# Optimization experiments

Hardware: AMD Instinct MI355X
Metric: run time of the kernel (lower is better)

Reference implementation:

```python
import jax, jax.numpy as jnp
import numpy as np

B, S, D = 8, 2048, 512
EPS = float(jnp.finfo(jnp.float32).eps)  # torch RMSNorm eps=None -> finfo eps


def rmsnorm(x, w):
    var = jnp.mean(jnp.square(x), axis=-1, keepdims=True)
    return x * jax.lax.rsqrt(var + EPS) * w


def setup_inputs() -> dict:
    key = jax.random.key(0)
    ks = jax.random.split(key, 9)
    x = jax.random.normal(ks[0], (B, S, D), dtype=jnp.float32)
    q_expl = jax.random.normal(ks[1], (B, S, D), dtype=jnp.float32)
    k_expl = jax.random.normal(ks[2], (B, S, D), dtype=jnp.float32)
    # parameters (torch Linear: y = x @ W^T + b; store W already transposed [in, out])
    sc1 = 1.0 / np.sqrt(D)
    W1 = jax.random.uniform(ks[3], (D, 2 * D), jnp.float32, -sc1, sc1)
    b1 = jax.random.uniform(ks[4], (2 * D,), jnp.float32, -sc1, sc1)
    W2 = jax.random.uniform(ks[5], (D, D), jnp.float32, -sc1, sc1)
    b2 = jax.random.uniform(ks[6], (D,), jnp.float32, -sc1, sc1)
    norm1_w = jnp.ones((D,), jnp.float32)
    norm2_w = jnp.ones((D,), jnp.float32)
    return {"x": x, "q_expl": q_expl, "k_expl": k_expl,
            "W1": W1, "b1": b1, "W2": W2, "b2": b2,
            "norm1_w": norm1_w, "norm2_w": norm2_w}


def reference(x, q_expl, k_expl, W1, b1, W2, b2, norm1_w, norm2_w):
    d = x.shape[-1]
    # single-head attention: scores [B,S,S]
    scores = jnp.einsum('bqd,bkd->bqk', q_expl, k_expl) / jnp.sqrt(jnp.float32(d))
    attn = jax.nn.softmax(scores, axis=-1)
    attn_out = jnp.einsum('bqk,bkd->bqd', attn, x)
    # dropout is identity in eval mode
    h = rmsnorm(x + attn_out, norm1_w)
    # GeGLU FFN: Linear(D->2D), chunk, gelu(x1)*x2, Linear(D->D)
    proj = h @ W1 + b1
    x1, x2 = jnp.split(proj, 2, axis=-1)
    g = jax.nn.gelu(x1, approximate=False) * x2
    ff = g @ W2 + b2
    return rmsnorm(h + ff, norm2_w)
```

## Files before the change

kernel.cpp:

```cpp
#include <hip/hip_runtime.h>
#include <math.h>

static constexpr float EPS_F = 1.1920929e-07f;
static constexpr float SCL   = 0.044194173824159216f;

typedef __attribute__((ext_vector_type(8))) short  short8;
typedef __attribute__((ext_vector_type(4))) float  floatx4;

__device__ __forceinline__ float4 ld4(const float* p){ return *(const float4*)p; }
__device__ __forceinline__ ushort f2bf(float f){
  union { float f; unsigned u; } v; v.f = f;
  return (ushort)((v.u + 0x7FFFu + ((v.u >> 16) & 1u)) >> 16);
}
__device__ __forceinline__ float bf2f(ushort h){
  union { unsigned u; float f; } v; v.u = ((unsigned)h) << 16;
  return v.f;
}
#define MFMA16(A,B,C) __builtin_amdgcn_mfma_f32_16x16x32_bf16((A),(B),(C),0,0,0)

__device__ __forceinline__ void gld16(void* lds, const void* g){
  __builtin_amdgcn_global_load_lds(
      (const __attribute__((address_space(1))) unsigned int*)g,
      (__attribute__((address_space(3))) unsigned int*)lds, 16, 0, 0);
}

__global__ __launch_bounds__(256)
void prep(const float* __restrict__ q, const float* __restrict__ k,
          const float* __restrict__ x, const float* __restrict__ W1,
          const float* __restrict__ W2,
          ushort* __restrict__ Qb, ushort* __restrict__ Kb,
          ushort* __restrict__ XT, ushort* __restrict__ W1T,
          ushort* __restrict__ W2T)
{
  const int bi = blockIdx.x, t = threadIdx.x;
  if (bi < 8192){
    const size_t i4 = ((size_t)bi*256 + t)*4;
    float4 v = ld4(q + i4);
    ushort4 o;
    o.x=f2bf(v.x*SCL); o.y=f2bf(v.y*SCL); o.z=f2bf(v.z*SCL); o.w=f2bf(v.w*SCL);
    *(ushort4*)(Qb + i4) = o;
    float4 u = ld4(k + i4);
    o.x=f2bf(u.x); o.y=f2bf(u.y); o.z=f2bf(u.z); o.w=f2bf(u.w);
    *(ushort4*)(Kb + i4) = o;
    return;
  }
  const float* in; ushort* out; int R, C, c0, r0; size_t boff;
  if (bi < 10240){
    const int id = bi - 8192;
    in = x; out = XT; R = 2048; C = 512;
    boff = (size_t)(id >> 8) * R * C;
    c0 = (id & 7)*64; r0 = ((id >> 3) & 31)*64;
  } else if (bi < 10368){
    const int id = bi - 10240;
    in = W1; out = W1T; R = 512; C = 1024; boff = 0;
    c0 = (id & 15)*64; r0 = (id >> 4)*64;
  } else {
    const int id = bi - 10368;
    in = W2; out = W2T; R = 512; C = 512; boff = 0;
    c0 = (id & 7)*64; r0 = (id >> 3)*64;
  }
  __shared__ __align__(16) ushort tile[64*68];
#pragma unroll
  for (int it = 0; it < 4; ++it){
    int f = t + it*256, r = f >> 4, c4 = f & 15;
    float4 v = ld4(in + boff + (size_t)(r0+r)*C + c0 + c4*4);
    ushort4 o; o.x=f2bf(v.x); o.y=f2bf(v.y); o.z=f2bf(v.z); o.w=f2bf(v.w);
    *(ushort4*)&tile[r*68 + c4*4] = o;
  }
  __syncthreads();
#pragma unroll
  for (int it = 0; it < 4; ++it){
    int f = t + it*256, c = f >> 4, q4 = f & 15;
    ushort4 o;
    o.x = tile[(q4*4+0)*68 + c];
    o.y = tile[(q4*4+1)*68 + c];
    o.z = tile[(q4*4+2)*68 + c];
    o.w = tile[(q4*4+3)*68 + c];
    *(ushort4*)(out + boff + (size_t)(c0+c)*R + r0 + q4*4) = o;
  }
}

__global__ __launch_bounds__(512)
void qk8(const ushort* __restrict__ Qbf, const ushort* __restrict__ Kbf,
         ushort* __restrict__ scores, float* __restrict__ rowsum)
{
  extern __shared__ __align__(16) ushort smem[];
  const int t = threadIdx.x, lane = t & 63, w = t >> 6;
  const int id = blockIdx.x;
  const int b = id & 7, s = id >> 3;
  const int m0 = (s & 7) * 256, n0 = (s >> 3) * 256;
  const ushort* Qb = Qbf + ((size_t)b*2048 + (size_t)m0)*512;
  const ushort* Kb = Kbf + ((size_t)b*2048 + (size_t)n0)*512;
  const int wr = w >> 2, wc = w & 3;
  const int l15 = lane & 15, quad = lane >> 4;
  const int c0  = (quad ^ (l15 & 7)) * 8;
  const int srow = lane >> 3;
  const int skc  = ((lane & 7) ^ srow) * 8;

  floatx4 acc[8][4];
#pragma unroll
  for (int i = 0; i < 8; ++i)
#pragma unroll
    for (int j = 0; j < 4; ++j) acc[i][j] = (floatx4){0.f,0.f,0.f,0.f};

  auto stage = [&](int buf, const ushort* gsrc, int isB, int kt, int h){
    ushort* base = smem + buf*32768 + isB*16384 + h*8192;
#pragma unroll
    for (int r = 0; r < 2; ++r){
      const int rw = r*8 + w;
      gld16(base + rw*512,
            gsrc + (size_t)(h*128 + rw*8 + srow)*512 + kt*64 + skc);
    }
  };

  stage(0, Qb, 0, 0, 0);
  stage(0, Qb, 0, 0, 1);
  stage(0, Kb, 1, 0, 0);
  stage(0, Kb, 1, 0, 1);
  stage(1, Kb, 1, 1, 0);
  stage(1, Kb, 1, 1, 1);
  asm volatile("s_waitcnt vmcnt(4)" ::: "memory");
  __builtin_amdgcn_s_barrier();

  short8 af[2][2], bfr[4][2];
  const int NT = 8;

  for (int kt = 0; kt < NT; ++kt){
    const int cur = kt & 1;
    const ushort* A  = smem + cur*32768;
    const ushort* Bt = A + 16384;
#pragma unroll
    for (int p = 0; p < 4; ++p){
      if (p == 0){
#pragma unroll
        for (int ni = 0; ni < 4; ++ni)
#pragma unroll
          for (int ks = 0; ks < 2; ++ks)
            bfr[ni][ks] = *(const short8*)
              &Bt[(wc*64 + ni*16 + l15)*64 + (c0 ^ (ks*32))];
      }
#pragma unroll
      for (int mi = 0; mi < 2; ++mi)
#pragma unroll
        for (int ks = 0; ks < 2; ++ks)
          af[mi][ks] = *(const short8*)
            &A[(wr*128 + (p*2 + mi)*16 + l15)*64 + (c0 ^ (ks*32))];
      if (p == 0 && kt+1 < NT) stage(cur^1, Qb, 0, kt+1, 0);
      if (p == 1 && kt+1 < NT) stage(cur^1, Qb, 0, kt+1, 1);
      if (p == 2 && kt+2 < NT) stage(cur,   Kb, 1, kt+2, 0);
      if (p == 3 && kt+2 < NT) stage(cur,   Kb, 1, kt+2, 1);
      __builtin_amdgcn_s_barrier();
      asm volatile("s_waitcnt lgkmcnt(0)" ::: "memory");
      __builtin_amdgcn_sched_barrier(0);
      __builtin_amdgcn_s_setprio(1);
#pragma unroll
      for (int mi = 0; mi < 2; ++mi)
#pragma unroll
        for (int ni = 0; ni < 4; ++ni)
#pragma unroll
          for (int ks = 0; ks < 2; ++ks)
            acc[p*2+mi][ni] = MFMA16(af[mi][ks], bfr[ni][ks], acc[p*2+mi][ni]);
      __builtin_amdgcn_s_setprio(0);
      if (p == 3){
        if (kt + 2 < NT) asm volatile("s_waitcnt vmcnt(4)" ::: "memory");
        else             asm volatile("s_waitcnt vmcnt(0)" ::: "memory");
      }
      __builtin_amdgcn_s_barrier();
    }
  }

  ushort* sb = scores + (size_t)b*2048*2048;
#pragma unroll
  for (int m = 0; m < 8; ++m){
    const int rm = m0 + wr*128 + m*16 + quad*4;
    float rs[4] = {0.f,0.f,0.f,0.f};
#pragma unroll
    for (int n = 0; n < 4; ++n){
      const int cn = n0 + wc*64 + n*16 + l15;
#pragma unroll
      for (int r = 0; r < 4; ++r){
        float e = __expf(acc[m][n][r]);
        ushort eb = f2bf(e);
        sb[(size_t)(rm + r)*2048 + cn] = eb;
        rs[r] += bf2f(eb);
      }
    }
#pragma unroll
    for (int r = 0; r < 4; ++r){
      float p2 = rs[r];
      p2 += __shfl_xor(p2, 1); p2 += __shfl_xor(p2, 2);
      p2 += __shfl_xor(p2, 4); p2 += __shfl_xor(p2, 8);
      if (l15 == 0)
        atomicAdd(&rowsum[(size_t)b*2048 + rm + r], p2);
    }
  }
}

__global__ __launch_bounds__(256)
void pv128(const ushort* __restrict__ P, const ushort* __restrict__ XT,
           const float* __restrict__ rowsum, ushort* __restrict__ attn)
{
  __shared__ __align__(16) ushort As[2][128*32];
  __shared__ __align__(16) ushort Bs[2][128*32];
  const int t=threadIdx.x, lane=t&63, w=t>>6;
  const int id = blockIdx.x;
  const int b = id & 7, s = id >> 3;
  const int m0 = (s >> 2)*128, n0 = (s & 3)*128;
  const ushort* Pb = P  + ((size_t)b*2048 + m0)*2048;
  const ushort* Xb = XT + ((size_t)b*512  + n0)*2048;
  const int sr = w*32 + (lane>>2), sc = (lane&3)*8;
  const int ga=(w&1)*4, gb2=(w>>1)*4, l15=lane&15, quad=lane>>4;

  floatx4 acc[4][4];
#pragma unroll
  for (int i=0;i<4;++i)
#pragma unroll
    for (int j=0;j<4;++j) acc[i][j]=(floatx4){0.f,0.f,0.f,0.f};

  auto stage = [&](int buf, int k0){
    gld16(&As[buf][(w*32)*32],    Pb + (size_t)sr*2048      + k0 + sc);
    gld16(&As[buf][(w*32+16)*32], Pb + (size_t)(sr+16)*2048 + k0 + sc);
    gld16(&Bs[buf][(w*32)*32],    Xb + (size_t)sr*2048      + k0 + sc);
    gld16(&Bs[buf][(w*32+16)*32], Xb + (size_t)(sr+16)*2048 + k0 + sc);
  };

  stage(0, 0);
  for (int kc=0; kc<64; ++kc){
    __syncthreads();
    if (kc < 63) stage((kc+1)&1, (kc+1)*32);
    const ushort* A = As[kc&1];
    const ushort* B = Bs[kc&1];
    short8 af[4], bfr[4];
#pragma unroll
    for (int i=0;i<4;++i) af[i]  = *(const short8*)&A[((ga+i)*16 + l15)*32 + quad*8];
#pragma unroll
    for (int j=0;j<4;++j) bfr[j] = *(const short8*)&B[((gb2+j)*16 + l15)*32 + quad*8];
#pragma unroll
    for (int i=0;i<4;++i)
#pragma unroll
      for (int j=0;j<4;++j)
        acc[i][j] = MFMA16(af[i], bfr[j], acc[i][j]);
  }

  ushort* ab = attn + (size_t)b*2048*512;
#pragma unroll
  for (int i=0;i<4;++i){
    const int rm = m0 + (ga+i)*16 + quad*4;
    float inv[4];
#pragma unroll
    for (int r=0;r<4;++r)
      inv[r] = 1.0f / rowsum[(size_t)b*2048 + rm + r];
#pragma unroll
    for (int j=0;j<4;++j){
      const int cn = n0 + (gb2+j)*16 + l15;
#pragma unroll
      for (int r=0;r<4;++r)
        ab[(size_t)(rm+r)*512 + cn] = f2bf(acc[i][j][r] * inv[r]);
    }
  }
}

__global__ __launch_bounds__(256)
void res_rms1(const float* __restrict__ x, const float* __restrict__ n1w,
              ushort* __restrict__ ah)
{
  const int wid = threadIdx.x >> 6, lane = threadIdx.x & 63;
  const size_t row = (size_t)blockIdx.x*4 + wid;
  ushort* ar = ah + row*512;
  const float* xr = x + row*512;
  ushort4 a0 = *(const ushort4*)&ar[lane*8];
  ushort4 a1 = *(const ushort4*)&ar[lane*8 + 4];
  float4 x0 = ld4(xr + lane*8), x1 = ld4(xr + lane*8 + 4);
  float h[8];
  h[0]=x0.x+bf2f(a0.x); h[1]=x0.y+bf2f(a0.y); h[2]=x0.z+bf2f(a0.z); h[3]=x0.w+bf2f(a0.w);
  h[4]=x1.x+bf2f(a1.x); h[5]=x1.y+bf2f(a1.y); h[6]=x1.z+bf2f(a1.z); h[7]=x1.w+bf2f(a1.w);
  float ss = 0.f;
#pragma unroll
  for (int e=0;e<8;++e) ss += h[e]*h[e];
#pragma unroll
  for (int s=1;s<64;s<<=1) ss += __shfl_xor(ss, s);
  const float rr = rsqrtf(ss*(1.0f/512.0f) + EPS_F);
  ushort4 o0, o1;
  o0.x=f2bf(h[0]*rr*n1w[lane*8+0]); o0.y=f2bf(h[1]*rr*n1w[lane*8+1]);
  o0.z=f2bf(h[2]*rr*n1w[lane*8+2]); o0.w=f2bf(h[3]*rr*n1w[lane*8+3]);
  o1.x=f2bf(h[4]*rr*n1w[lane*8+4]); o1.y=f2bf(h[5]*rr*n1w[lane*8+5]);
  o1.z=f2bf(h[6]*rr*n1w[lane*8+6]); o1.w=f2bf(h[7]*rr*n1w[lane*8+7]);
  *(ushort4*)&ar[lane*8]     = o0;
  *(ushort4*)&ar[lane*8 + 4] = o1;
}

__global__ __launch_bounds__(256)
void ffn1(const ushort* __restrict__ hbf, const ushort* __restrict__ W1T,
          const float* __restrict__ b1, ushort* __restrict__ gbuf)
{
  __shared__ __align__(16) ushort As[2][128*32];
  __shared__ __align__(16) ushort Bs[2][128*32];
  const int t=threadIdx.x, lane=t&63, w=t>>6;
  const int id = blockIdx.x;
  const int xcd = id & 7, sl = id >> 3;
  const int m0 = (xcd*16 + (sl>>3))*128, n0 = (sl & 7)*64;
  const int sr = w*32 + (lane>>2), sc=(lane&3)*8;
  const int ga=(w&1)*4, b2w=(w>>1);
  const int l15=lane&15, quad=lane>>4;
  const int gr0 = (sr < 64) ? (n0+sr) : (448+n0+sr);
  const int sr1 = sr+16;
  const int gr1 = (sr1 < 64) ? (n0+sr1) : (448+n0+sr1);

  floatx4 acc[4][4];
#pragma unroll
  for (int i=0;i<4;++i)
#pragma unroll
    for (int j=0;j<4;++j) acc[i][j]=(floatx4){0.f,0.f,0.f,0.f};

  auto stage = [&](int buf, int k0){
    gld16(&As[buf][(w*32)*32],    hbf + (size_t)(m0+sr)*512  + k0 + sc);
    gld16(&As[buf][(w*32+16)*32], hbf + (size_t)(m0+sr1)*512 + k0 + sc);
    gld16(&Bs[buf][(w*32)*32],    W1T + (size_t)gr0*512 + k0 + sc);
    gld16(&Bs[buf][(w*32+16)*32], W1T + (size_t)gr1*512 + k0 + sc);
  };

  stage(0, 0);
  for (int kc=0; kc<16; ++kc){
    __syncthreads();
    if (kc < 15) stage((kc+1)&1, (kc+1)*32);
    const ushort* A = As[kc&1];
    const ushort* B = Bs[kc&1];
    short8 af[4], bfr[4];
#pragma unroll
    for (int i=0;i<4;++i) af[i] = *(const short8*)&A[((ga+i)*16 + l15)*32 + quad*8];
#pragma unroll
    for (int jj=0;jj<4;++jj){
      const int g1 = (jj<2) ? (b2w*2+jj) : (4 + b2w*2 + (jj-2));
      bfr[jj] = *(const short8*)&B[(g1*16 + l15)*32 + quad*8];
    }
#pragma unroll
    for (int i=0;i<4;++i)
#pragma unroll
      for (int jj=0;jj<4;++jj)
        acc[i][jj] = MFMA16(af[i], bfr[jj], acc[i][jj]);
  }

#pragma unroll
  for (int i=0;i<4;++i){
#pragma unroll
    for (int jj=0;jj<2;++jj){
      const int col = n0 + (b2w*2+jj)*16 + l15;
      const float bb1 = b1[col], bb2 = b1[512+col];
#pragma unroll
      for (int r=0;r<4;++r){
        const int row = m0 + (ga+i)*16 + quad*4 + r;
        float x1 = acc[i][jj][r]   + bb1;
        float x2 = acc[i][jj+2][r] + bb2;
        float gl = 0.5f*x1*(1.0f + erff(x1*0.70710678118654752f));
        gbuf[(size_t)row*512 + col] = f2bf(gl*x2);
      }
    }
  }
}

__global__ __launch_bounds__(256)
void ff128(const ushort* __restrict__ gb, const ushort* __restrict__ W2T,
           ushort* __restrict__ ff)
{
  __shared__ __align__(16) ushort As[2][128*32];
  __shared__ __align__(16) ushort Bs[2][128*32];
  const int t=threadIdx.x, lane=t&63, w=t>>6;
  const int id = blockIdx.x;
  const int xcd = id & 7, sl = id >> 3;
  const int m0 = (xcd*16 + (sl>>2))*128, n0 = (sl & 3)*128;
  const ushort* Ab = gb  + (size_t)m0*512;
  const ushort* Bb = W2T + (size_t)n0*512;
  const int sr = w*32 + (lane>>2), sc = (lane&3)*8;
  const int ga=(w&1)*4, gb2=(w>>1)*4, l15=lane&15, quad=lane>>4;

  floatx4 acc[4][4];
#pragma unroll
  for (int i=0;i<4;++i)
#pragma unroll
    for (int j=0;j<4;++j) acc[i][j]=(floatx4){0.f,0.f,0.f,0.f};

  auto stage = [&](int buf, int k0){
    gld16(&As[buf][(w*32)*32],    Ab + (size_t)sr*512      + k0 + sc);
    gld16(&As[buf][(w*32+16)*32], Ab + (size_t)(sr+16)*512 + k0 + sc);
    gld16(&Bs[buf][(w*32)*32],    Bb + (size_t)sr*512      + k0 + sc);
    gld16(&Bs[buf][(w*32+16)*32], Bb + (size_t)(sr+16)*512 + k0 + sc);
  };

  stage(0, 0);
  for (int kc=0; kc<16; ++kc){
    __syncthreads();
    if (kc < 15) stage((kc+1)&1, (kc+1)*32);
    const ushort* A = As[kc&1];
    const ushort* B = Bs[kc&1];
    short8 af[4], bfr[4];
#pragma unroll
    for (int i=0;i<4;++i) af[i]  = *(const short8*)&A[((ga+i)*16 + l15)*32 + quad*8];
#pragma unroll
    for (int j=0;j<4;++j) bfr[j] = *(const short8*)&B[((gb2+j)*16 + l15)*32 + quad*8];
#pragma unroll
    for (int i=0;i<4;++i)
#pragma unroll
      for (int j=0;j<4;++j)
        acc[i][j] = MFMA16(af[i], bfr[j], acc[i][j]);
  }

#pragma unroll
  for (int i=0;i<4;++i){
    const int rm = m0 + (ga+i)*16 + quad*4;
#pragma unroll
    for (int j=0;j<4;++j){
      const int cn = n0 + (gb2+j)*16 + l15;
#pragma unroll
      for (int r=0;r<4;++r)
        ff[(size_t)(rm+r)*512 + cn] = f2bf(acc[i][j][r]);
    }
  }
}

__global__ __launch_bounds__(256)
void res_rms2(const ushort* __restrict__ hbf, const ushort* __restrict__ ff,
              const float* __restrict__ b2, const float* __restrict__ n2w,
              float* __restrict__ out)
{
  const int wid = threadIdx.x >> 6, lane = threadIdx.x & 63;
  const size_t row = (size_t)blockIdx.x*4 + wid;
  const ushort* hr = hbf + row*512;
  const ushort* fr = ff  + row*512;
  ushort4 h0 = *(const ushort4*)&hr[lane*8];
  ushort4 h1 = *(const ushort4*)&hr[lane*8 + 4];
  ushort4 f0 = *(const ushort4*)&fr[lane*8];
  ushort4 f1 = *(const ushort4*)&fr[lane*8 + 4];
  float4 bb0 = ld4(b2 + lane*8), bb1 = ld4(b2 + lane*8 + 4);
  float y[8];
  y[0]=bf2f(h0.x)+bf2f(f0.x)+bb0.x; y[1]=bf2f(h0.y)+bf2f(f0.y)+bb0.y;
  y[2]=bf2f(h0.z)+bf2f(f0.z)+bb0.z; y[3]=bf2f(h0.w)+bf2f(f0.w)+bb0.w;
  y[4]=bf2f(h1.x)+bf2f(f1.x)+bb1.x; y[5]=bf2f(h1.y)+bf2f(f1.y)+bb1.y;
  y[6]=bf2f(h1.z)+bf2f(f1.z)+bb1.z; y[7]=bf2f(h1.w)+bf2f(f1.w)+bb1.w;
  float ss = 0.f;
#pragma unroll
  for (int e=0;e<8;++e) ss += y[e]*y[e];
#pragma unroll
  for (int s=1;s<64;s<<=1) ss += __shfl_xor(ss, s);
  const float rr = rsqrtf(ss*(1.0f/512.0f) + EPS_F);
  float4 w0 = ld4(n2w + lane*8), w1 = ld4(n2w + lane*8 + 4);
  float* orow = out + row*512;
  float4 o0, o1;
  o0.x=y[0]*rr*w0.x; o0.y=y[1]*rr*w0.y; o0.z=y[2]*rr*w0.z; o0.w=y[3]*rr*w0.w;
  o1.x=y[4]*rr*w1.x; o1.y=y[5]*rr*w1.y; o1.z=y[6]*rr*w1.z; o1.w=y[7]*rr*w1.w;
  *(float4*)(orow + lane*8)     = o0;
  *(float4*)(orow + lane*8 + 4) = o1;
}

extern "C" void kernel_launch(void* const* d_in, const int* in_sizes, int n_in,
                              void* d_out, int out_size, void* d_ws, size_t ws_size,
                              hipStream_t stream)
{
  const float* x   = (const float*)d_in[0];
  const float* q   = (const float*)d_in[1];
  const float* k   = (const float*)d_in[2];
  const float* W1  = (const float*)d_in[3];
  const float* b1  = (const float*)d_in[4];
  const float* W2  = (const float*)d_in[5];
  const float* b2  = (const float*)d_in[6];
  const float* n1w = (const float*)d_in[7];
  const float* n2w = (const float*)d_in[8];
  float* out = (float*)d_out;

  ushort* scoresP = (ushort*)d_ws;
  ushort* XT  = scoresP + (size_t)8*2048*2048;
  ushort* Qbf = XT  + (size_t)8*512*2048;
  ushort* Kbf = Qbf + (size_t)8*2048*512;
  ushort* W1T = Kbf + (size_t)8*2048*512;
  ushort* W2T = W1T + (size_t)1024*512;
  float*  rowsum = (float*)(W2T + (size_t)512*512);
  ushort* attn = Qbf;
  ushort* hbf  = Qbf;
  ushort* gbuf = Kbf;
  ushort* ffb  = scoresP;

  hipMemsetAsync(rowsum, 0, (size_t)8*2048*sizeof(float), stream);
  prep     <<<dim3(10432),  256, 0, stream>>>(q, k, x, W1, W2, Qbf, Kbf, XT, W1T, W2T);
  qk8      <<<dim3(512),    512, 131072, stream>>>(Qbf, Kbf, scoresP, rowsum);
  pv128    <<<dim3(512),    256, 0, stream>>>(scoresP, XT, rowsum, attn);
  res_rms1 <<<dim3(4096),   256, 0, stream>>>(x, n1w, hbf);
  ffn1     <<<dim3(1024),   256, 0, stream>>>(hbf, W1T, b1, gbuf);
  ff128    <<<dim3(512),    256, 0, stream>>>(gbuf, W2T, ffb);
  res_rms2 <<<dim3(4096),   256, 0, stream>>>(hbf, ffb, b2, n2w, out);
}
```

Before: 324.9 us.

## Rewrite PV GEMM with 256x128 tiles, 8 warps, swizzled LDS and split pipeline

Replaces the 128x128, 4-warp PV kernel with a 256x128-tile, 8-warp kernel. It uses 64-wide k-steps, XOR-swizzled shared memory to avoid bank conflicts, and a multi-stage pipeline that staggers A-half and B loads between two MFMA phases, using explicit waitcnt, barriers and setprio. The aim is to raise data reuse per block and overlap global-to-LDS loads with matrix math. The cost is 96KB of LDS per block and only 256 blocks, which lowers occupancy. It also relies on delicate manual synchronisation.

```diff
diff --git a/kernel.cpp b/kernel.cpp
--- a/kernel.cpp
+++ b/kernel.cpp
@@ -196,66 +196,130 @@
   }
 }
 
-__global__ __launch_bounds__(256)
-void pv128(const ushort* __restrict__ P, const ushort* __restrict__ XT,
-           const float* __restrict__ rowsum, ushort* __restrict__ attn)
-{
-  __shared__ __align__(16) ushort As[2][128*32];
-  __shared__ __align__(16) ushort Bs[2][128*32];
-  const int t=threadIdx.x, lane=t&63, w=t>>6;
+__global__ __launch_bounds__(512)
+void pv8(const ushort* __restrict__ P, const ushort* __restrict__ XT,
+         const float* __restrict__ rowsum, ushort* __restrict__ attn)
+{
+  extern __shared__ __align__(16) ushort smem[];
+  const int t = threadIdx.x, lane = t & 63, w = t >> 6;
   const int id = blockIdx.x;
   const int b = id & 7, s = id >> 3;
-  const int m0 = (s >> 2)*128, n0 = (s & 3)*128;
+  const int m0 = (s >> 2) * 256;
+  const int n0 = (s & 3) * 128;
   const ushort* Pb = P  + ((size_t)b*2048 + m0)*2048;
   const ushort* Xb = XT + ((size_t)b*512  + n0)*2048;
-  const int sr = w*32 + (lane>>2), sc = (lane&3)*8;
-  const int ga=(w&1)*4, gb2=(w>>1)*4, l15=lane&15, quad=lane>>4;
+  const int wr = w >> 1, wc = w & 1;
+  const int l15 = lane & 15, quad = lane >> 4;
+  const int c0  = (quad ^ (l15 & 7)) * 8;
+  const int srow = lane >> 3;
+  const int skc  = ((lane & 7) ^ srow) * 8;
 
   floatx4 acc[4][4];
 #pragma unroll
-  for (int i=0;i<4;++i)
-#pragma unroll
-    for (int j=0;j<4;++j) acc[i][j]=(floatx4){0.f,0.f,0.f,0.f};
-
-  auto stage = [&](int buf, int k0){
-    gld16(&As[buf][(w*32)*32],    Pb + (size_t)sr*2048      + k0 + sc);
-    gld16(&As[buf][(w*32+16)*32], Pb + (size_t)(sr+16)*2048 + k0 + sc);
-    gld16(&Bs[buf][(w*32)*32],    Xb + (size_t)sr*2048      + k0 + sc);
-    gld16(&Bs[buf][(w*32+16)*32], Xb + (size_t)(sr+16)*2048 + k0 + sc);
+  for (int i = 0; i < 4; ++i)
+#pragma unroll
+    for (int j = 0; j < 4; ++j) acc[i][j] = (floatx4){0.f,0.f,0.f,0.f};
+
+  auto stageA = [&](int buf, int kt, int h){
+    ushort* base = smem + buf*24576 + h*8192;
+#pragma unroll
+    for (int r = 0; r < 2; ++r){
+      const int rw = r*8 + w;
+      gld16(base + rw*512,
+            Pb + (size_t)(h*128 + rw*8 + srow)*2048 + kt*64 + skc);
+    }
   };
-
-  stage(0, 0);
-  for (int kc=0; kc<64; ++kc){
-    __syncthreads();
-    if (kc < 63) stage((kc+1)&1, (kc+1)*32);
-    const ushort* A = As[kc&1];
-    const ushort* B = Bs[kc&1];
-    short8 af[4], bfr[4];
-#pragma unroll
-    for (int i=0;i<4;++i) af[i]  = *(const short8*)&A[((ga+i)*16 + l15)*32 + quad*8];
-#pragma unroll
-    for (int j=0;j<4;++j) bfr[j] = *(const short8*)&B[((gb2+j)*16 + l15)*32 + quad*8];
-#pragma unroll
-    for (int i=0;i<4;++i)
-#pragma unroll
-      for (int j=0;j<4;++j)
-        acc[i][j] = MFMA16(af[i], bfr[j], acc[i][j]);
+  auto stageB = [&](int buf, int kt){
+    ushort* base = smem + buf*24576 + 16384;
+#pragma unroll
+    for (int r = 0; r < 2; ++r){
+      const int rw = r*8 + w;
+      gld16(base + rw*512,
+            Xb + (size_t)(rw*8 + srow)*2048 + kt*64 + skc);
+    }
+  };
+
+  stageA(0, 0, 0);
+  stageA(0, 0, 1);
+  stageB(0, 0);
+  stageB(1, 1);
+  asm volatile("s_waitcnt vmcnt(2)" ::: "memory");
+  __builtin_amdgcn_s_barrier();
+
+  short8 af[2][2], bfr[4][2];
+  const int NT = 32;
+
+  for (int kt = 0; kt < NT; ++kt){
+    const int cur = kt & 1;
+    const ushort* A  = smem + cur*24576;
+    const ushort* Bt = A + 16384;
+
+#pragma unroll
+    for (int ni = 0; ni < 4; ++ni)
+#pragma unroll
+      for (int ks = 0; ks < 2; ++ks)
+        bfr[ni][ks] = *(const short8*)
+          &Bt[(wc*64 + ni*16 + l15)*64 + (c0 ^ (ks*32))];
+#pragma unroll
+    for (int mi = 0; mi < 2; ++mi)
+#pragma unroll
+      for (int ks = 0; ks < 2; ++ks)
+        af[mi][ks] = *(const short8*)
+          &A[(wr*64 + mi*16 + l15)*64 + (c0 ^ (ks*32))];
+    if (kt+1 < NT) stageA(cur^1, kt+1, 0);
+    __builtin_amdgcn_s_barrier();
+    asm volatile("s_waitcnt lgkmcnt(0)" ::: "memory");
+    __builtin_amdgcn_sched_barrier(0);
+    __builtin_amdgcn_s_setprio(1);
+#pragma unroll
+    for (int mi = 0; mi < 2; ++mi)
+#pragma unroll
+      for (int ni = 0; ni < 4; ++ni)
+#pragma unroll
+        for (int ks = 0; ks < 2; ++ks)
+          acc[mi][ni] = MFMA16(af[mi][ks], bfr[ni][ks], acc[mi][ni]);
+    __builtin_amdgcn_s_setprio(0);
+    __builtin_amdgcn_s_barrier();
+
+#pragma unroll
+    for (int mi = 0; mi < 2; ++mi)
+#pragma unroll
+      for (int ks = 0; ks < 2; ++ks)
+        af[mi][ks] = *(const short8*)
+          &A[(wr*64 + (2+mi)*16 + l15)*64 + (c0 ^ (ks*32))];
+    if (kt+1 < NT) stageA(cur^1, kt+1, 1);
+    if (kt+2 < NT) stageB(cur, kt+2);
+    __builtin_amdgcn_s_barrier();
+    asm volatile("s_waitcnt lgkmcnt(0)" ::: "memory");
+    __builtin_amdgcn_sched_barrier(0);
+    __builtin_amdgcn_s_setprio(1);
+#pragma unroll
+    for (int mi = 0; mi < 2; ++mi)
+#pragma unroll
+      for (int ni = 0; ni < 4; ++ni)
+#pragma unroll
+        for (int ks = 0; ks < 2; ++ks)
+          acc[2+mi][ni] = MFMA16(af[mi][ks], bfr[ni][ks], acc[2+mi][ni]);
+    __builtin_amdgcn_s_setprio(0);
+    if (kt + 2 < NT) asm volatile("s_waitcnt vmcnt(2)" ::: "memory");
+    else             asm volatile("s_waitcnt vmcnt(0)" ::: "memory");
+    __builtin_amdgcn_s_barrier();
   }
 
   ushort* ab = attn + (size_t)b*2048*512;
 #pragma unroll
-  for (int i=0;i<4;++i){
-    const int rm = m0 + (ga+i)*16 + quad*4;
+  for (int m = 0; m < 4; ++m){
+    const int rm = m0 + wr*64 + m*16 + quad*4;
     float inv[4];
 #pragma unroll
-    for (int r=0;r<4;++r)
+    for (int r = 0; r < 4; ++r)
       inv[r] = 1.0f / rowsum[(size_t)b*2048 + rm + r];
 #pragma unroll
-    for (int j=0;j<4;++j){
-      const int cn = n0 + (gb2+j)*16 + l15;
-#pragma unroll
-      for (int r=0;r<4;++r)
-        ab[(size_t)(rm+r)*512 + cn] = f2bf(acc[i][j][r] * inv[r]);
+    for (int n = 0; n < 4; ++n){
+      const int cn = n0 + wc*64 + n*16 + l15;
+#pragma unroll
+      for (int r = 0; r < 4; ++r)
+        ab[(size_t)(rm + r)*512 + cn] = f2bf(acc[m][n][r] * inv[r]);
     }
   }
 }
@@ -481,7 +545,7 @@
   hipMemsetAsync(rowsum, 0, (size_t)8*2048*sizeof(float), stream);
   prep     <<<dim3(10432),  256, 0, stream>>>(q, k, x, W1, W2, Qbf, Kbf, XT, W1T, W2T);
   qk8      <<<dim3(512),    512, 131072, stream>>>(Qbf, Kbf, scoresP, rowsum);
-  pv128    <<<dim3(512),    256, 0, stream>>>(scoresP, XT, rowsum, attn);
+  pv8      <<<dim3(256),    512,  98304, stream>>>(scoresP, XT, rowsum, attn);
   res_rms1 <<<dim3(4096),   256, 0, stream>>>(x, n1w, hbf);
   ffn1     <<<dim3(1024),   256, 0, stream>>>(hbf, W1T, b1, gbuf);
   ff128    <<<dim3(512),    256, 0, stream>>>(gbuf, W2T, ffb);
```

New measurement: 315.6 us. -2.9%, faster.
